# Performance work log

Hardware: AMD Instinct MI355X
Metric: run time of the kernel (lower is better)

Reference implementation:

```python
import jax, jax.numpy as jnp
import numpy as np
import math

EMBED = 512
HEADS = 2
HEAD_DIM = EMBED // HEADS
EPS = 1e-5

def layer_norm(x, g, b):
    mu = jnp.mean(x, axis=-1, keepdims=True)
    var = jnp.var(x, axis=-1, keepdims=True)
    return (x - mu) * jax.lax.rsqrt(var + EPS) * g + b

def setup_inputs() -> dict:
    key = jax.random.key(0)
    ks = jax.random.split(key, 16)
    s = 0.02
    inp = {
        "text_embeds": jax.random.normal(ks[0], (128, 32, EMBED), jnp.float32),
        "video_embeds": jax.random.normal(ks[1], (64, 12, EMBED), jnp.float32),
        "ln1_g": jnp.ones((EMBED,), jnp.float32),
        "ln1_b": jnp.zeros((EMBED,), jnp.float32),
        "Wq": jax.random.normal(ks[2], (EMBED, EMBED), jnp.float32) * s,
        "bq": jnp.zeros((EMBED,), jnp.float32),
        "Wk": jax.random.normal(ks[3], (EMBED, EMBED), jnp.float32) * s,
        "bk": jnp.zeros((EMBED,), jnp.float32),
        "Wv": jax.random.normal(ks[4], (EMBED, EMBED), jnp.float32) * s,
        "bv": jnp.zeros((EMBED,), jnp.float32),
        "Wo": jax.random.normal(ks[5], (EMBED, EMBED), jnp.float32) * s,
        "bo": jnp.zeros((EMBED,), jnp.float32),
        "Wl": jax.random.normal(ks[6], (EMBED, EMBED), jnp.float32) * s,
        "bl": jnp.zeros((EMBED,), jnp.float32),
        "ln2_g": jnp.ones((EMBED,), jnp.float32),
        "ln2_b": jnp.zeros((EMBED,), jnp.float32),
        "ln3_g": jnp.ones((EMBED,), jnp.float32),
        "ln3_b": jnp.zeros((EMBED,), jnp.float32),
    }
    return inp

def reference(text_embeds, video_embeds, ln1_g, ln1_b, Wq, bq, Wk, bk, Wv, bv,
              Wo, bo, Wl, bl, ln2_g, ln2_b, ln3_g, ln3_b):
    # shared layer_norm1 on both modalities
    t = layer_norm(text_embeds, ln1_g, ln1_b)    # [T, Nw, E]
    vd = layer_norm(video_embeds, ln1_g, ln1_b)  # [V, F, E]
    T, Nw, _ = t.shape
    V, Fr, _ = vd.shape
    q = (t @ Wq.T + bq).reshape(T, Nw, HEADS, HEAD_DIM)   # bthd
    k = (vd @ Wk.T + bk).reshape(V, Fr, HEADS, HEAD_DIM)  # avhd
    v = (vd @ Wv.T + bv).reshape(V, Fr, HEADS, HEAD_DIM)  # avhd
    # cross-modal outer-product attention logits: [V, T, H, F, Nw]
    logits = jnp.einsum('avhd,bthd->abhvt', k, q) / math.sqrt(HEAD_DIM)
    weights = jax.nn.softmax(logits, axis=3)  # softmax over frames
    attn = jnp.einsum('avhd,abhvt->abhtd', v, weights)  # [V, T, H, Nw, D]
    attn = attn.transpose(0, 1, 3, 2, 4).reshape(V, T, Nw, EMBED)
    attn = attn.mean(axis=0)                    # [T, Nw, E]
    o = attn @ Wo.T + bo
    o = layer_norm(o, ln2_g, ln2_b)
    lin = o @ Wl.T + bl  # dropout is identity in eval mode
    out = layer_norm(o + lin, ln3_g, ln3_b)
    return out
```

## Files before the change

kernel.cpp:

```cpp
#include <hip/hip_runtime.h>
#include <math.h>

#define EMBED 512
#define HD 256
#define FR 12
#define NV 64
#define NT_TOK 4096
#define NV_TOK 768

typedef __attribute__((ext_vector_type(8))) short short8;
typedef __attribute__((ext_vector_type(4))) float f32x4;

__device__ __forceinline__ unsigned int f2bf(float f) {
  unsigned int u = __float_as_uint(f);
  u += 0x7FFFu + ((u >> 16) & 1u);
  return u >> 16;
}
__device__ __forceinline__ float bf2f(unsigned int h) {
  return __uint_as_float(h << 16);
}
__device__ __forceinline__ void async_cp16(void* lds, const void* g) {
  __builtin_amdgcn_global_load_lds(
      (const __attribute__((address_space(1))) void*)g,
      (__attribute__((address_space(3))) void*)lds, 16, 0, 0);
}

__device__ __forceinline__ void gemm_core(
    const unsigned short* __restrict__ Ab, int lda,
    const unsigned short* __restrict__ Bb, int ldb,
    int m0, int n0, int K,
    unsigned short* As, unsigned short* Bs, f32x4 acc[4][2]) {
  int tid = threadIdx.x;
  int w = tid >> 6, lane = tid & 63;
  int lr = lane & 15, quad = lane >> 4;
  int wm = (w >> 1) * 64, wn = (w & 1) * 32;
  int rowA[4], cgA[4], rowB[2], cgB[2];
  #pragma unroll
  for (int i = 0; i < 4; ++i) {
    int s = tid + i * 256;
    rowA[i] = s >> 3;
    cgA[i] = (s & 7) ^ (rowA[i] & 7);
  }
  #pragma unroll
  for (int i = 0; i < 2; ++i) {
    int s = tid + i * 256;
    rowB[i] = s >> 3;
    cgB[i] = (s & 7) ^ (rowB[i] & 7);
  }
  for (int k0 = 0; k0 < K; k0 += 64) {
    __syncthreads();
    #pragma unroll
    for (int i = 0; i < 4; ++i)
      async_cp16(&As[(tid + i * 256) * 8],
                 Ab + (size_t)(m0 + rowA[i]) * lda + k0 + cgA[i] * 8);
    #pragma unroll
    for (int i = 0; i < 2; ++i)
      async_cp16(&Bs[(tid + i * 256) * 8],
                 Bb + (size_t)(n0 + rowB[i]) * ldb + k0 + cgB[i] * 8);
    __syncthreads();
    #pragma unroll
    for (int kk = 0; kk < 2; ++kk) {
      int sw = ((kk * 4 + quad) ^ (lr & 7)) * 8;
      short8 b0 = *(const short8*)&Bs[(wn + lr) * 64 + sw];
      short8 b1 = *(const short8*)&Bs[(wn + 16 + lr) * 64 + sw];
      #pragma unroll
      for (int i = 0; i < 4; ++i) {
        short8 a = *(const short8*)&As[(wm + i * 16 + lr) * 64 + sw];
        acc[i][0] = __builtin_amdgcn_mfma_f32_16x16x32_bf16(a, b0, acc[i][0], 0, 0, 0);
        acc[i][1] = __builtin_amdgcn_mfma_f32_16x16x32_bf16(a, b1, acc[i][1], 0, 0, 0);
      }
    }
  }
}

template <bool OUT_BF, bool BIAS>
__global__ __launch_bounds__(256) void gemm128(
    const unsigned short* __restrict__ A, int lda, long AzS,
    const unsigned short* __restrict__ B, int ldb, long BzS,
    const float* __restrict__ bias, void* __restrict__ Cv, int ldc, long CzS,
    int K) {
  __shared__ __align__(16) unsigned short As[128 * 64];
  __shared__ __align__(16) unsigned short Bs[64 * 64];
  f32x4 acc[4][2] = {};
  const unsigned short* Ab = A + (size_t)blockIdx.z * AzS;
  const unsigned short* Bb = B + (size_t)blockIdx.z * BzS;
  int m0 = blockIdx.x * 128, n0 = blockIdx.y * 64;
  gemm_core(Ab, lda, Bb, ldb, m0, n0, K, As, Bs, acc);
  int w = threadIdx.x >> 6, lane = threadIdx.x & 63;
  int lr = lane & 15, quad = lane >> 4;
  int wm = (w >> 1) * 64, wn = (w & 1) * 32;
  long cz = (long)blockIdx.z * CzS;
  #pragma unroll
  for (int j = 0; j < 2; ++j) {
    int col = n0 + wn + j * 16 + lr;
    float bv = BIAS ? bias[col] : 0.0f;
    #pragma unroll
    for (int i = 0; i < 4; ++i) {
      int rbase = m0 + wm + i * 16 + quad * 4;
      #pragma unroll
      for (int r = 0; r < 4; ++r) {
        float v = acc[i][j][r] + bv;
        if (OUT_BF)
          ((unsigned short*)Cv)[cz + (size_t)(rbase + r) * ldc + col] =
              (unsigned short)f2bf(v);
        else
          ((float*)Cv)[cz + (size_t)(rbase + r) * ldc + col] = v;
      }
    }
  }
}

__global__ __launch_bounds__(256) void qkv_kernel(
    const unsigned short* __restrict__ tn, const unsigned short* __restrict__ vn,
    const unsigned short* __restrict__ Wq, const unsigned short* __restrict__ Wk,
    const unsigned short* __restrict__ Wv,
    const float* __restrict__ bq, const float* __restrict__ bk,
    const float* __restrict__ bv,
    unsigned short* __restrict__ Q, unsigned short* __restrict__ Kout,
    unsigned short* __restrict__ Vt) {
  __shared__ __align__(16) unsigned short As[128 * 64];
  __shared__ __align__(16) unsigned short Bs[64 * 64];
  int bid = blockIdx.x;
  const unsigned short *Ap, *Bp;
  const float* bias;
  unsigned short* outp = nullptr;
  int m0, n0, mode;
  if (bid < 256) {
    Ap = tn; Bp = Wq; bias = bq; outp = Q;
    m0 = (bid >> 3) * 128; n0 = (bid & 7) * 64; mode = 0;
  } else if (bid < 304) {
    int i = bid - 256;
    Ap = vn; Bp = Wk; bias = bk; outp = Kout;
    m0 = (i >> 3) * 128; n0 = (i & 7) * 64; mode = 0;
  } else {
    int i = bid - 304;
    Ap = vn; Bp = Wv; bias = bv;
    m0 = (i >> 3) * 128; n0 = (i & 7) * 64; mode = 1;
  }
  f32x4 acc[4][2] = {};
  gemm_core(Ap, EMBED, Bp, EMBED, m0, n0, EMBED, As, Bs, acc);
  int w = threadIdx.x >> 6, lane = threadIdx.x & 63;
  int lr = lane & 15, quad = lane >> 4;
  int wm = (w >> 1) * 64, wn = (w & 1) * 32;
  #pragma unroll
  for (int j = 0; j < 2; ++j) {
    int col = n0 + wn + j * 16 + lr;
    float bvv = bias[col];
    #pragma unroll
    for (int i = 0; i < 4; ++i) {
      int rbase = m0 + wm + i * 16 + quad * 4;
      if (mode == 0) {
        #pragma unroll
        for (int r = 0; r < 4; ++r)
          outp[(size_t)(rbase + r) * EMBED + col] =
              (unsigned short)f2bf(acc[i][j][r] + bvv);
      } else {
        ushort4 pk;
        pk.x = (unsigned short)f2bf(acc[i][j][0] + bvv);
        pk.y = (unsigned short)f2bf(acc[i][j][1] + bvv);
        pk.z = (unsigned short)f2bf(acc[i][j][2] + bvv);
        pk.w = (unsigned short)f2bf(acc[i][j][3] + bvv);
        *(ushort4*)&Vt[(size_t)col * NV_TOK + rbase] = pk;
      }
    }
  }
}

__device__ __forceinline__ void ln_row(
    const float* __restrict__ xr, const float* __restrict__ rr,
    const float* __restrict__ g, const float* __restrict__ b,
    float* __restrict__ outf, unsigned short* __restrict__ outb) {
  int t = threadIdx.x;
  float v0 = xr[t], v1 = xr[t + 256];
  if (rr != nullptr) { v0 += rr[t]; v1 += rr[t + 256]; }
  float s = v0 + v1;
  float s2 = v0 * v0 + v1 * v1;
  #pragma unroll
  for (int off = 32; off > 0; off >>= 1) {
    s += __shfl_down(s, off, 64);
    s2 += __shfl_down(s2, off, 64);
  }
  __shared__ float ss[4], ss2[4];
  __shared__ float mean_s, rstd_s;
  int wid = t >> 6;
  if ((t & 63) == 0) { ss[wid] = s; ss2[wid] = s2; }
  __syncthreads();
  if (t == 0) {
    float a = ss[0] + ss[1] + ss[2] + ss[3];
    float a2 = ss2[0] + ss2[1] + ss2[2] + ss2[3];
    float mean = a * (1.0f / EMBED);
    float var = a2 * (1.0f / EMBED) - mean * mean;
    mean_s = mean;
    rstd_s = rsqrtf(var + 1e-5f);
  }
  __syncthreads();
  float mean = mean_s, rstd = rstd_s;
  float y0 = (v0 - mean) * rstd * g[t] + b[t];
  float y1 = (v1 - mean) * rstd * g[t + 256] + b[t + 256];
  if (outf != nullptr) { outf[t] = y0; outf[t + 256] = y1; }
  if (outb != nullptr) {
    outb[t] = (unsigned short)f2bf(y0);
    outb[t + 256] = (unsigned short)f2bf(y1);
  }
}

__global__ __launch_bounds__(256) void ln_kernel(
    const float* __restrict__ x, const float* __restrict__ res,
    const float* __restrict__ g, const float* __restrict__ b,
    float* __restrict__ outf, unsigned short* __restrict__ outb) {
  size_t row = blockIdx.x;
  ln_row(x + row * EMBED, res ? res + row * EMBED : nullptr, g, b,
         outf ? outf + row * EMBED : nullptr,
         outb ? outb + row * EMBED : nullptr);
}

__global__ __launch_bounds__(256) void prep_kernel(
    const float* __restrict__ text, const float* __restrict__ video,
    const float* __restrict__ g, const float* __restrict__ b,
    const float* __restrict__ Wq, const float* __restrict__ Wk,
    const float* __restrict__ Wv, const float* __restrict__ Wo,
    const float* __restrict__ Wl, unsigned short* __restrict__ Wbf,
    unsigned short* __restrict__ tn, unsigned short* __restrict__ vn) {
  int bid = blockIdx.x;
  if (bid < 1280) {
    int i = bid * 256 + threadIdx.x;
    const float* srcs[5] = {Wq, Wk, Wv, Wo, Wl};
    const float* src = srcs[i >> 16];
    float4 v = ((const float4*)src)[i & 65535];
    uint2 o;
    o.x = f2bf(v.x) | (f2bf(v.y) << 16);
    o.y = f2bf(v.z) | (f2bf(v.w) << 16);
    ((uint2*)Wbf)[i] = o;
    return;
  }
  if (bid < 1280 + NT_TOK) {
    size_t row = bid - 1280;
    ln_row(text + row * EMBED, nullptr, g, b, nullptr, tn + row * EMBED);
  } else {
    size_t row = bid - (1280 + NT_TOK);
    ln_row(video + row * EMBED, nullptr, g, b, nullptr, vn + row * EMBED);
  }
}

__global__ __launch_bounds__(256) void softmax12_kernel(unsigned short* __restrict__ S) {
  int gi = blockIdx.x * 256 + threadIdx.x;
  uint2* p = (uint2*)(S + (size_t)gi * 12);
  uint2 u0 = p[0], u1 = p[1], u2 = p[2];
  float v[12];
  v[0] = bf2f(u0.x & 0xffff); v[1] = bf2f(u0.x >> 16);
  v[2] = bf2f(u0.y & 0xffff); v[3] = bf2f(u0.y >> 16);
  v[4] = bf2f(u1.x & 0xffff); v[5] = bf2f(u1.x >> 16);
  v[6] = bf2f(u1.y & 0xffff); v[7] = bf2f(u1.y >> 16);
  v[8] = bf2f(u2.x & 0xffff); v[9] = bf2f(u2.x >> 16);
  v[10] = bf2f(u2.y & 0xffff); v[11] = bf2f(u2.y >> 16);
  float m = -1e30f;
  #pragma unroll
  for (int f = 0; f < FR; ++f) { v[f] *= 0.0625f; m = fmaxf(m, v[f]); }
  float s = 0.f;
  #pragma unroll
  for (int f = 0; f < FR; ++f) { v[f] = __expf(v[f] - m); s += v[f]; }
  float inv = (1.0f / NV) / s;
  unsigned int w[12];
  #pragma unroll
  for (int f = 0; f < FR; ++f) w[f] = f2bf(v[f] * inv);
  uint2 o0, o1, o2;
  o0.x = w[0] | (w[1] << 16);  o0.y = w[2] | (w[3] << 16);
  o1.x = w[4] | (w[5] << 16);  o1.y = w[6] | (w[7] << 16);
  o2.x = w[8] | (w[9] << 16);  o2.y = w[10] | (w[11] << 16);
  p[0] = o0; p[1] = o1; p[2] = o2;
}

extern "C" void kernel_launch(void* const* d_in, const int* in_sizes, int n_in,
                              void* d_out, int out_size, void* d_ws, size_t ws_size,
                              hipStream_t stream) {
  (void)in_sizes; (void)n_in; (void)out_size; (void)ws_size;
  const float* text  = (const float*)d_in[0];
  const float* video = (const float*)d_in[1];
  const float* ln1_g = (const float*)d_in[2];
  const float* ln1_b = (const float*)d_in[3];
  const float* Wq = (const float*)d_in[4];
  const float* bq = (const float*)d_in[5];
  const float* Wk = (const float*)d_in[6];
  const float* bk = (const float*)d_in[7];
  const float* Wv = (const float*)d_in[8];
  const float* bv = (const float*)d_in[9];
  const float* Wo = (const float*)d_in[10];
  const float* bo = (const float*)d_in[11];
  const float* Wl = (const float*)d_in[12];
  const float* bl = (const float*)d_in[13];
  const float* ln2_g = (const float*)d_in[14];
  const float* ln2_b = (const float*)d_in[15];
  const float* ln3_g = (const float*)d_in[16];
  const float* ln3_b = (const float*)d_in[17];
  float* out = (float*)d_out;

  char* base = (char*)d_ws;
  unsigned short* Wbf   = (unsigned short*)base;
  unsigned short* Wq_bf = Wbf + 0 * 262144;
  unsigned short* Wk_bf = Wbf + 1 * 262144;
  unsigned short* Wv_bf = Wbf + 2 * 262144;
  unsigned short* Wo_bf = Wbf + 3 * 262144;
  unsigned short* Wl_bf = Wbf + 4 * 262144;
  unsigned short* Vt    = (unsigned short*)(base + 2621440);
  char* big = base + 3407872;
  unsigned short* Q_bf   = (unsigned short*)(big + 0);
  unsigned short* K_bf   = (unsigned short*)(big + 4194304);
  unsigned short* S      = (unsigned short*)(big + 4980736);
  unsigned short* tn_bf  = (unsigned short*)(big + 17563648);
  unsigned short* vn_bf  = (unsigned short*)(big + 21757952);
  unsigned short* att_bf = (unsigned short*)(big + 17563648);
  float*          Ob     = (float*)(big + 4980736);
  float*          o2f    = (float*)(big + 13369344);
  unsigned short* o2_bf  = (unsigned short*)(big + 21757952);
  float*          lin    = (float*)(big + 0);

  prep_kernel<<<1280 + NT_TOK + NV_TOK, 256, 0, stream>>>(
      text, video, ln1_g, ln1_b, Wq, Wk, Wv, Wo, Wl, Wbf, tn_bf, vn_bf);

  qkv_kernel<<<352, 256, 0, stream>>>(tn_bf, vn_bf, Wq_bf, Wk_bf, Wv_bf,
                                      bq, bk, bv, Q_bf, K_bf, Vt);

  gemm128<true, false><<<dim3(32, 12, 2), 256, 0, stream>>>(
      Q_bf, EMBED, HD, K_bf, EMBED, HD, nullptr, S, NV_TOK,
      (long)NT_TOK * NV_TOK, HD);
  softmax12_kernel<<<2048, 256, 0, stream>>>(S);
  gemm128<true, false><<<dim3(32, 4, 2), 256, 0, stream>>>(
      S, NV_TOK, (long)NT_TOK * NV_TOK, Vt, NV_TOK, (long)HD * NV_TOK, nullptr,
      att_bf, EMBED, HD, NV_TOK);

  gemm128<false, true><<<dim3(32, 8, 1), 256, 0, stream>>>(
      att_bf, EMBED, 0, Wo_bf, EMBED, 0, bo, Ob, EMBED, 0, EMBED);
  ln_kernel<<<NT_TOK, 256, 0, stream>>>(Ob, nullptr, ln2_g, ln2_b, o2f, o2_bf);
  gemm128<false, true><<<dim3(32, 8, 1), 256, 0, stream>>>(
      o2_bf, EMBED, 0, Wl_bf, EMBED, 0, bl, lin, EMBED, 0, EMBED);
  ln_kernel<<<NT_TOK, 256, 0, stream>>>(o2f, lin, ln3_g, ln3_b, out, nullptr);
}
```

Measured before the change: 176.2 us.

## Double-buffer GEMM LDS tiles with async prefetch and stage softmax through LDS

The shared GEMM core now double-buffers its A and B tiles in LDS. It issues the async global-to-LDS loads for the next K slice before computing on the current one, and uses raw barriers with vmcnt waits instead of two __syncthreads per iteration, so memory latency can overlap the MFMA work. LDS use per block doubles, which may lower occupancy. Separately, the softmax kernel now stages its rows through LDS so that its global reads and writes are coalesced, rather than each thread doing strided 24-byte accesses.

```diff
diff --git a/kernel.cpp b/kernel.cpp
--- a/kernel.cpp
+++ b/kernel.cpp
@@ -8,6 +8,9 @@
 #define NT_TOK 4096
 #define NV_TOK 768
 
+#define WAIT_VM6 0x0F76
+#define WAIT_VM0 0x0F70
+
 typedef __attribute__((ext_vector_type(8))) short short8;
 typedef __attribute__((ext_vector_type(4))) float f32x4;
 
@@ -29,7 +32,8 @@
     const unsigned short* __restrict__ Ab, int lda,
     const unsigned short* __restrict__ Bb, int ldb,
     int m0, int n0, int K,
-    unsigned short* As, unsigned short* Bs, f32x4 acc[4][2]) {
+    unsigned short* __restrict__ As, unsigned short* __restrict__ Bs,
+    f32x4 acc[4][2]) {
   int tid = threadIdx.x;
   int w = tid >> 6, lane = tid & 63;
   int lr = lane & 15, quad = lane >> 4;
@@ -38,34 +42,51 @@
   #pragma unroll
   for (int i = 0; i < 4; ++i) {
     int s = tid + i * 256;
-    rowA[i] = s >> 3;
-    cgA[i] = (s & 7) ^ (rowA[i] & 7);
+    rowA[i] = s >> 3; cgA[i] = (s & 7) ^ (rowA[i] & 7);
   }
   #pragma unroll
   for (int i = 0; i < 2; ++i) {
     int s = tid + i * 256;
-    rowB[i] = s >> 3;
-    cgB[i] = (s & 7) ^ (rowB[i] & 7);
-  }
-  for (int k0 = 0; k0 < K; k0 += 64) {
-    __syncthreads();
-    #pragma unroll
-    for (int i = 0; i < 4; ++i)
-      async_cp16(&As[(tid + i * 256) * 8],
-                 Ab + (size_t)(m0 + rowA[i]) * lda + k0 + cgA[i] * 8);
-    #pragma unroll
-    for (int i = 0; i < 2; ++i)
-      async_cp16(&Bs[(tid + i * 256) * 8],
-                 Bb + (size_t)(n0 + rowB[i]) * ldb + k0 + cgB[i] * 8);
-    __syncthreads();
+    rowB[i] = s >> 3; cgB[i] = (s & 7) ^ (rowB[i] & 7);
+  }
+  int nk = K >> 6;
+  #pragma unroll
+  for (int i = 0; i < 4; ++i)
+    async_cp16(&As[(tid + i * 256) * 8],
+               Ab + (size_t)(m0 + rowA[i]) * lda + cgA[i] * 8);
+  #pragma unroll
+  for (int i = 0; i < 2; ++i)
+    async_cp16(&Bs[(tid + i * 256) * 8],
+               Bb + (size_t)(n0 + rowB[i]) * ldb + cgB[i] * 8);
+  for (int k = 0; k < nk; ++k) {
+    int cur = k & 1;
+    __builtin_amdgcn_s_barrier();
+    if (k + 1 < nk) {
+      int nxt = cur ^ 1;
+      int koff = (k + 1) << 6;
+      #pragma unroll
+      for (int i = 0; i < 4; ++i)
+        async_cp16(&As[nxt * 8192 + (tid + i * 256) * 8],
+                   Ab + (size_t)(m0 + rowA[i]) * lda + koff + cgA[i] * 8);
+      #pragma unroll
+      for (int i = 0; i < 2; ++i)
+        async_cp16(&Bs[nxt * 4096 + (tid + i * 256) * 8],
+                   Bb + (size_t)(n0 + rowB[i]) * ldb + koff + cgB[i] * 8);
+      __builtin_amdgcn_s_waitcnt(WAIT_VM6);
+    } else {
+      __builtin_amdgcn_s_waitcnt(WAIT_VM0);
+    }
+    __builtin_amdgcn_s_barrier();
+    const unsigned short* Ac = As + cur * 8192;
+    const unsigned short* Bc = Bs + cur * 4096;
     #pragma unroll
     for (int kk = 0; kk < 2; ++kk) {
       int sw = ((kk * 4 + quad) ^ (lr & 7)) * 8;
-      short8 b0 = *(const short8*)&Bs[(wn + lr) * 64 + sw];
-      short8 b1 = *(const short8*)&Bs[(wn + 16 + lr) * 64 + sw];
+      short8 b0 = *(const short8*)&Bc[(wn + lr) * 64 + sw];
+      short8 b1 = *(const short8*)&Bc[(wn + 16 + lr) * 64 + sw];
       #pragma unroll
       for (int i = 0; i < 4; ++i) {
-        short8 a = *(const short8*)&As[(wm + i * 16 + lr) * 64 + sw];
+        short8 a = *(const short8*)&Ac[(wm + i * 16 + lr) * 64 + sw];
         acc[i][0] = __builtin_amdgcn_mfma_f32_16x16x32_bf16(a, b0, acc[i][0], 0, 0, 0);
         acc[i][1] = __builtin_amdgcn_mfma_f32_16x16x32_bf16(a, b1, acc[i][1], 0, 0, 0);
       }
@@ -79,8 +100,8 @@
     const unsigned short* __restrict__ B, int ldb, long BzS,
     const float* __restrict__ bias, void* __restrict__ Cv, int ldc, long CzS,
     int K) {
-  __shared__ __align__(16) unsigned short As[128 * 64];
-  __shared__ __align__(16) unsigned short Bs[64 * 64];
+  __shared__ __align__(16) unsigned short As[2 * 128 * 64];
+  __shared__ __align__(16) unsigned short Bs[2 * 64 * 64];
   f32x4 acc[4][2] = {};
   const unsigned short* Ab = A + (size_t)blockIdx.z * AzS;
   const unsigned short* Bb = B + (size_t)blockIdx.z * BzS;
@@ -118,8 +139,8 @@
     const float* __restrict__ bv,
     unsigned short* __restrict__ Q, unsigned short* __restrict__ Kout,
     unsigned short* __restrict__ Vt) {
-  __shared__ __align__(16) unsigned short As[128 * 64];
-  __shared__ __align__(16) unsigned short Bs[64 * 64];
+  __shared__ __align__(16) unsigned short As[2 * 128 * 64];
+  __shared__ __align__(16) unsigned short Bs[2 * 64 * 64];
   int bid = blockIdx.x;
   const unsigned short *Ap, *Bp;
   const float* bias;
@@ -243,9 +264,13 @@
 }
 
 __global__ __launch_bounds__(256) void softmax12_kernel(unsigned short* __restrict__ S) {
-  int gi = blockIdx.x * 256 + threadIdx.x;
-  uint2* p = (uint2*)(S + (size_t)gi * 12);
-  uint2 u0 = p[0], u1 = p[1], u2 = p[2];
+  __shared__ uint2 buf[768];
+  int t = threadIdx.x;
+  uint2* g = (uint2*)S + (size_t)blockIdx.x * 768;
+  #pragma unroll
+  for (int i = 0; i < 3; ++i) buf[t + i * 256] = g[t + i * 256];
+  __syncthreads();
+  uint2 u0 = buf[t * 3], u1 = buf[t * 3 + 1], u2 = buf[t * 3 + 2];
   float v[12];
   v[0] = bf2f(u0.x & 0xffff); v[1] = bf2f(u0.x >> 16);
   v[2] = bf2f(u0.y & 0xffff); v[3] = bf2f(u0.y >> 16);
@@ -267,7 +292,10 @@
   o0.x = w[0] | (w[1] << 16);  o0.y = w[2] | (w[3] << 16);
   o1.x = w[4] | (w[5] << 16);  o1.y = w[6] | (w[7] << 16);
   o2.x = w[8] | (w[9] << 16);  o2.y = w[10] | (w[11] << 16);
-  p[0] = o0; p[1] = o1; p[2] = o2;
+  buf[t * 3] = o0; buf[t * 3 + 1] = o1; buf[t * 3 + 2] = o2;
+  __syncthreads();
+  #pragma unroll
+  for (int i = 0; i < 3; ++i) g[t + i * 256] = buf[t + i * 256];
 }
 
 extern "C" void kernel_launch(void* const* d_in, const int* in_sizes, int n_in,
```

Measured after the change: 171.4 us. -2.8%, faster.
